# Optimization experiments

Hardware: AMD Instinct MI355X
Metric: run time of the kernel (lower is better)

The kernel has to match this reference:

```python
import jax, jax.numpy as jnp
import numpy as np

EMBED = 512
KDIM = 512
VDIM = 512
HEADS = 8
DHEAD = EMBED // HEADS  # 64
SCALE = 1.0 / np.sqrt(DHEAD).astype(np.float32)


def setup_inputs() -> dict:
    key = jax.random.key(0)
    ks = jax.random.split(key, 11)
    B, Lq, Lk = 4, 2048, 2048
    s_in = 1.0 / np.sqrt(EMBED).astype(np.float32)
    return {
        "query": jax.random.normal(ks[0], (B, Lq, EMBED), jnp.float32),
        "key": jax.random.normal(ks[1], (B, Lk, KDIM), jnp.float32),
        "value": jax.random.normal(ks[2], (B, Lk, VDIM), jnp.float32),
        "wq": jax.random.normal(ks[3], (EMBED, KDIM), jnp.float32) * s_in,
        "bq": jnp.zeros((KDIM,), jnp.float32),
        "wk": jax.random.normal(ks[4], (KDIM, KDIM), jnp.float32) * s_in,
        "bk": jnp.zeros((KDIM,), jnp.float32),
        "wv": jax.random.normal(ks[5], (VDIM, VDIM), jnp.float32) * s_in,
        "bv": jnp.zeros((VDIM,), jnp.float32),
        "wo": jax.random.normal(ks[6], (VDIM, EMBED), jnp.float32) * s_in,
        "bo": jnp.zeros((EMBED,), jnp.float32),
    }


def _split_heads(x):
    b, l, _ = x.shape
    return x.reshape(b, l, HEADS, DHEAD).transpose(0, 2, 1, 3)  # b h l d


def reference(query, key, value, wq, bq, wk, bk, wv, bv, wo, bo):
    # Linear projections (weights stored [in, out])
    q = _split_heads(query @ wq + bq)   # b h Lq d
    k = _split_heads(key @ wk + bk)     # b h Lk d
    v = _split_heads(value @ wv + bv)   # b h Lk d
    scores = jnp.einsum('bhid,bhjd->bhij', q, k) * SCALE  # b h Lq Lk
    attn = jax.nn.softmax(scores, axis=-1)
    # dropout is identity in eval mode
    ctx = jnp.einsum('bhij,bhjd->bhid', attn, v)  # b h Lq d
    b, h, l, d = ctx.shape
    ctx = ctx.transpose(0, 2, 1, 3).reshape(b, l, h * d)  # b Lq vdim
    return ctx @ wo + bo
```

## Files before the change

### kernel.cpp

```cpp
#include <hip/hip_runtime.h>
#include <stdint.h>

typedef unsigned short u16;
typedef unsigned int u32;
typedef __attribute__((ext_vector_type(8))) short short8;
typedef __attribute__((ext_vector_type(4))) float f32x4;
typedef __attribute__((ext_vector_type(16))) float f32x16;

#define DEVI static __device__ __forceinline__

DEVI u16 f2bf(float f) {
  union { float f; u32 u; } v; v.f = f;
  u32 r = v.u + 0x7FFFu + ((v.u >> 16) & 1u);
  return (u16)(r >> 16);
}

DEVI u32 pack2bf(float lo, float hi) {
  return (u32)f2bf(lo) | ((u32)f2bf(hi) << 16);
}

DEVI u32 pack2bf_fast(float lo, float hi) {
  union { float f; u32 u; } a, b;
  a.f = lo; b.f = hi;
  return __builtin_amdgcn_perm(b.u + 0x8000u, a.u + 0x8000u, 0x07060302u);
}

DEVI u32 sum2bf(u32 a, u32 b, float sc) {
  union { u32 u; float f; } alo, ahi, blo, bhi;
  alo.u = a << 16; ahi.u = a & 0xFFFF0000u;
  blo.u = b << 16; bhi.u = b & 0xFFFF0000u;
  return pack2bf_fast((alo.f + blo.f) * sc, (ahi.f + bhi.f) * sc);
}

DEVI void gload_lds16(const u16* g, u16* l) {
  __builtin_amdgcn_global_load_lds((const __attribute__((address_space(1))) void*)g,
                                   (__attribute__((address_space(3))) void*)l, 16, 0, 0);
}

DEVI int sw8(int chunk, int r) { return ((chunk ^ (r & 7) ^ ((r >> 3) & 3)) * 8); }

__global__ __launch_bounds__(256) void tw4(const float* __restrict__ s0, const float* __restrict__ s1,
                                           const float* __restrict__ s2, const float* __restrict__ s3,
                                           u16* __restrict__ d0, u16* __restrict__ d1,
                                           u16* __restrict__ d2, u16* __restrict__ d3) {
  int z = blockIdx.z;
  const float* src = z == 0 ? s0 : z == 1 ? s1 : z == 2 ? s2 : s3;
  u16* dst = z == 0 ? d0 : z == 1 ? d1 : z == 2 ? d2 : d3;
  __shared__ float tile[32][33];
  int tx = threadIdx.x & 31, ty = threadIdx.x >> 5;
  int bx = blockIdx.x * 32, by = blockIdx.y * 32;
#pragma unroll
  for (int i = 0; i < 32; i += 8)
    tile[ty + i][tx] = src[(size_t)(by + ty + i) * 512 + bx + tx];
  __syncthreads();
#pragma unroll
  for (int i = 0; i < 32; i += 8)
    dst[(size_t)(bx + ty + i) * 512 + by + tx] = f2bf(tile[tx][ty + i]);
}

__global__ __launch_bounds__(256) void gemm_qkv(
    const float* __restrict__ A0, const float* __restrict__ A1, const float* __restrict__ A2,
    const u16* __restrict__ W0, const u16* __restrict__ W1, const u16* __restrict__ W2,
    const float* __restrict__ b0, const float* __restrict__ b1, const float* __restrict__ b2,
    u16* __restrict__ oq, u16* __restrict__ ok, u16* __restrict__ vt, float qscale) {
  const int z = blockIdx.z;
  const float* A = z == 0 ? A0 : z == 1 ? A1 : A2;
  const u16* WT = z == 0 ? W0 : z == 1 ? W1 : W2;
  const float* bias = z == 0 ? b0 : z == 1 ? b1 : b2;
  const float sc = z == 0 ? qscale : 1.0f;

  __shared__ __align__(16) u16 smem[128 * 64 * 2];
  u16* As = smem;
  u16* Bs = smem + 128 * 64;
  const int t = threadIdx.x;
  const int w = t >> 6, lane = t & 63, quad = lane >> 4, li = lane & 15;
  const int flat = blockIdx.x + (blockIdx.y << 2);
  const int xcd = flat & 7, idx = flat >> 3;
  const int m0 = (((idx >> 2) << 3) + xcd) * 128;
  const int n0 = (idx & 3) * 128;
  const int wm = (w >> 1) * 64, wn = (w & 1) * 64;

  f32x4 zv = {0.f, 0.f, 0.f, 0.f};
  f32x4 acc[4][4];
#pragma unroll
  for (int mi = 0; mi < 4; mi++)
#pragma unroll
    for (int ni = 0; ni < 4; ni++) acc[mi][ni] = zv;

  const int rA = t >> 3, cA = t & 7;
  for (int it = 0; it < 8; it++) {
    const int k0 = it * 64;
#pragma unroll
    for (int p = 0; p < 4; p++) {
      int r = p * 32 + rA;
      const float* ga = A + (size_t)(m0 + r) * 512 + k0 + cA * 8;
      float4 f0 = *(const float4*)ga;
      float4 f1 = *(const float4*)(ga + 4);
      uint4 pk;
      pk.x = pack2bf_fast(f0.x, f0.y);
      pk.y = pack2bf_fast(f0.z, f0.w);
      pk.z = pack2bf_fast(f1.x, f1.y);
      pk.w = pack2bf_fast(f1.z, f1.w);
      *(uint4*)&As[r * 64 + sw8(cA, r)] = pk;
    }
#pragma unroll
    for (int p = 0; p < 4; p++) {
      int s = p * 256 + t;
      int r = s >> 3, c8 = s & 7;
      gload_lds16(WT + (size_t)(n0 + r) * 512 + k0 + sw8(c8, r), &Bs[(p * 256 + w * 64) * 8]);
    }
    __syncthreads();
#pragma unroll
    for (int ks = 0; ks < 2; ks++) {
      short8 af[4], bf[4];
#pragma unroll
      for (int mi = 0; mi < 4; mi++) {
        int r = wm + mi * 16 + li;
        af[mi] = *(const short8*)&As[r * 64 + sw8(ks * 4 + quad, r)];
      }
#pragma unroll
      for (int ni = 0; ni < 4; ni++) {
        int r = wn + ni * 16 + li;
        bf[ni] = *(const short8*)&Bs[r * 64 + sw8(ks * 4 + quad, r)];
      }
#pragma unroll
      for (int mi = 0; mi < 4; mi++)
#pragma unroll
        for (int ni = 0; ni < 4; ni++)
          acc[mi][ni] = __builtin_amdgcn_mfma_f32_16x16x32_bf16(af[mi], bf[ni], acc[mi][ni], 0, 0, 0);
    }
    __syncthreads();
  }

  float bv[4];
#pragma unroll
  for (int ni = 0; ni < 4; ni++) bv[ni] = bias[n0 + wn + ni * 16 + li];

  if (z < 2) {
    u16* out = z == 0 ? oq : ok;
#pragma unroll
    for (int mi = 0; mi < 4; mi++)
#pragma unroll
      for (int ni = 0; ni < 4; ni++)
#pragma unroll
        for (int r = 0; r < 4; r++) {
          int row = m0 + wm + mi * 16 + quad * 4 + r;
          int col = n0 + wn + ni * 16 + li;
          out[(size_t)row * 512 + col] = f2bf((acc[mi][ni][r] + bv[ni]) * sc);
        }
  } else {
    u16* LT = smem;
#pragma unroll
    for (int mi = 0; mi < 4; mi++)
#pragma unroll
      for (int ni = 0; ni < 4; ni++) {
        int col = wn + ni * 16 + li;
        int row0 = wm + mi * 16 + quad * 4;
        uint2 dw;
        dw.x = pack2bf(acc[mi][ni][0] + bv[ni], acc[mi][ni][1] + bv[ni]);
        dw.y = pack2bf(acc[mi][ni][2] + bv[ni], acc[mi][ni][3] + bv[ni]);
        *(uint2*)&LT[col * 128 + (row0 ^ ((col & 7) << 3))] = dw;
      }
    __syncthreads();
    const int rr = t >> 1, half = t & 1;
    const int colg = n0 + rr;
    const int h = colg >> 6, dd = colg & 63;
    const int bb = m0 >> 11, l0 = m0 & 2047;
    u16* gdst = vt + ((size_t)((bb * 8 + h) * 64 + dd)) * 2048 + l0 + half * 64;
#pragma unroll
    for (int c = 0; c < 8; c++) {
      short8 v = *(const short8*)&LT[rr * 128 + half * 64 + ((c ^ (rr & 7)) << 3)];
      *(short8*)(gdst + c * 8) = v;
    }
  }
}

__global__ __launch_bounds__(256) void gemm_out(const u16* __restrict__ O0,
                                                const u16* __restrict__ O1,
                                                const float* __restrict__ Lb,
                                                const u16* __restrict__ WT,
                                                const float* __restrict__ bias,
                                                float* __restrict__ out) {
  __shared__ __align__(16) u16 As[128 * 64];
  __shared__ __align__(16) u16 Bs[64 * 64];
  __shared__ float Linv[8 * 128];
  const int t = threadIdx.x;
  const int w = t >> 6, lane = t & 63, quad = lane >> 4, li = lane & 15;
  const int flat = blockIdx.x + (blockIdx.y << 3);
  const int xcd = flat & 7, idx = flat >> 3;
  const int m0 = (((idx >> 3) << 3) + xcd) * 128;
  const int n0 = (idx & 7) * 64;
  const int wm = (w >> 1) * 64, wn = (w & 1) * 32;
  const int bb = m0 >> 11, qb = m0 & 2047;

#pragma unroll
  for (int j = 0; j < 4; j++) {
    int f2 = t + j * 256;
    int hh = f2 >> 7, qq = f2 & 127;
    float l0v = Lb[((size_t)((bb * 8 + hh) * 2 + 0)) * 2048 + qb + qq];
    float l1v = Lb[((size_t)((bb * 8 + hh) * 2 + 1)) * 2048 + qb + qq];
    Linv[f2] = 1.0f / (l0v + l1v);
  }
  __syncthreads();

  f32x4 zv = {0.f, 0.f, 0.f, 0.f};
  f32x4 acc[4][2];
#pragma unroll
  for (int mi = 0; mi < 4; mi++)
#pragma unroll
    for (int ni = 0; ni < 2; ni++) acc[mi][ni] = zv;

  const int rA = t >> 3, cA = t & 7;
  for (int it = 0; it < 8; it++) {
    const int k0 = it * 64;
#pragma unroll
    for (int p = 0; p < 4; p++) {
      int r = p * 32 + rA;
      size_t off = (size_t)(m0 + r) * 512 + k0 + cA * 8;
      uint4 a0 = *(const uint4*)&O0[off];
      uint4 a1 = *(const uint4*)&O1[off];
      float scq = Linv[it * 128 + r];
      uint4 pk;
      pk.x = sum2bf(a0.x, a1.x, scq);
      pk.y = sum2bf(a0.y, a1.y, scq);
      pk.z = sum2bf(a0.z, a1.z, scq);
      pk.w = sum2bf(a0.w, a1.w, scq);
      *(uint4*)&As[r * 64 + sw8(cA, r)] = pk;
    }
#pragma unroll
    for (int p = 0; p < 2; p++) {
      int s = p * 256 + t;
      int r = s >> 3, c8 = s & 7;
      gload_lds16(WT + (size_t)(n0 + r) * 512 + k0 + sw8(c8, r), &Bs[(p * 256 + w * 64) * 8]);
    }
    __syncthreads();
#pragma unroll
    for (int ks = 0; ks < 2; ks++) {
      short8 af[4], bf[2];
#pragma unroll
      for (int mi = 0; mi < 4; mi++) {
        int r = wm + mi * 16 + li;
        af[mi] = *(const short8*)&As[r * 64 + sw8(ks * 4 + quad, r)];
      }
#pragma unroll
      for (int ni = 0; ni < 2; ni++) {
        int r = wn + ni * 16 + li;
        bf[ni] = *(const short8*)&Bs[r * 64 + sw8(ks * 4 + quad, r)];
      }
#pragma unroll
      for (int mi = 0; mi < 4; mi++)
#pragma unroll
        for (int ni = 0; ni < 2; ni++)
          acc[mi][ni] = __builtin_amdgcn_mfma_f32_16x16x32_bf16(af[mi], bf[ni], acc[mi][ni], 0, 0, 0);
    }
    __syncthreads();
  }

  float bv[2];
#pragma unroll
  for (int ni = 0; ni < 2; ni++) bv[ni] = bias[n0 + wn + ni * 16 + li];
#pragma unroll
  for (int mi = 0; mi < 4; mi++)
#pragma unroll
    for (int ni = 0; ni < 2; ni++)
#pragma unroll
      for (int r = 0; r < 4; r++) {
        int row = m0 + wm + mi * 16 + quad * 4 + r;
        int col = n0 + wn + ni * 16 + li;
        out[(size_t)row * 512 + col] = acc[mi][ni][r] + bv[ni];
      }
}

__global__ __launch_bounds__(256, 4) void attn(const u16* __restrict__ Qp,
                                               const u16* __restrict__ Kp,
                                               const u16* __restrict__ VT,
                                               u16* __restrict__ Oq0,
                                               u16* __restrict__ Oq1,
                                               float* __restrict__ Lb) {
  __shared__ __align__(16) u16 Ks[64 * 64];
  __shared__ __align__(16) u16 Vs[64 * 64];
  __shared__ __align__(16) u16 Ps[4][32 * 64];
  const int t = threadIdx.x;
  const int w = t >> 6, lane = t & 63, qn = lane & 31, hi = lane >> 5;
  const int flat = blockIdx.x + (blockIdx.y << 4);
  const int xcd = flat & 7, idx = flat >> 3;
  const int g = ((idx >> 4) << 3) + xcd;
  const int h = g >> 1, s = g & 1;
  const int b = blockIdx.z;
  const int q0 = (idx & 15) * 128;
  const int qrow = q0 + w * 32 + qn;

  short8 qf[4];
  {
    const u16* qg = Qp + (size_t)(b * 2048 + qrow) * 512 + h * 64 + hi * 8;
#pragma unroll
    for (int ks = 0; ks < 4; ks++) qf[ks] = *(const short8*)(qg + ks * 16);
  }

  f32x16 o[2];
#pragma unroll
  for (int dt = 0; dt < 2; dt++)
#pragma unroll
    for (int r = 0; r < 16; r++) o[dt][r] = 0.f;
  float lsum = 0.f;

  u16* pw = &Ps[w][0];

  for (int kt = s * 16; kt < s * 16 + 16; kt++) {
    const int k0 = kt * 64;
#pragma unroll
    for (int i = 0; i < 2; i++) {
      int si = i * 256 + t;
      int r = si >> 3, c8 = si & 7;
      gload_lds16(Kp + (size_t)(b * 2048 + k0 + r) * 512 + h * 64 + sw8(c8, r),
                  &Ks[(i * 256 + w * 64) * 8]);
      gload_lds16(VT + ((size_t)((b * 8 + h) * 64 + r)) * 2048 + k0 + sw8(c8, r),
                  &Vs[(i * 256 + w * 64) * 8]);
    }
    __syncthreads();

    f32x16 st[2];
#pragma unroll
    for (int kjt = 0; kjt < 2; kjt++) {
#pragma unroll
      for (int r = 0; r < 16; r++) st[kjt][r] = 0.f;
#pragma unroll
      for (int ks = 0; ks < 4; ks++) {
        int m = kjt * 32 + qn;
        short8 ka = *(const short8*)&Ks[m * 64 + sw8(ks * 2 + hi, m)];
        st[kjt] = __builtin_amdgcn_mfma_f32_32x32x16_bf16(ka, qf[ks], st[kjt], 0, 0, 0);
      }
    }

#pragma unroll
    for (int kjt = 0; kjt < 2; kjt++)
#pragma unroll
      for (int k8 = 0; k8 < 4; k8++) {
        float p0 = __builtin_amdgcn_exp2f(st[kjt][k8 * 4 + 0]);
        float p1 = __builtin_amdgcn_exp2f(st[kjt][k8 * 4 + 1]);
        float p2 = __builtin_amdgcn_exp2f(st[kjt][k8 * 4 + 2]);
        float p3 = __builtin_amdgcn_exp2f(st[kjt][k8 * 4 + 3]);
        lsum += (p0 + p1) + (p2 + p3);
        uint2 dw;
        dw.x = pack2bf_fast(p0, p1);
        dw.y = pack2bf_fast(p2, p3);
        *(uint2*)&pw[qn * 64 + sw8(kjt * 4 + k8, qn) + hi * 4] = dw;
      }

    short8 pb[4];
#pragma unroll
    for (int ks = 0; ks < 4; ks++)
      pb[ks] = *(const short8*)&pw[qn * 64 + sw8(ks * 2 + hi, qn)];
#pragma unroll
    for (int dt = 0; dt < 2; dt++)
#pragma unroll
      for (int ks = 0; ks < 4; ks++) {
        int m = dt * 32 + qn;
        short8 va = *(const short8*)&Vs[m * 64 + sw8(ks * 2 + hi, m)];
        o[dt] = __builtin_amdgcn_mfma_f32_32x32x16_bf16(va, pb[ks], o[dt], 0, 0, 0);
      }
    __syncthreads();
  }

  float l = lsum + __shfl_xor(lsum, 32);
  if (hi == 0) Lb[((size_t)((b * 8 + h) * 2 + s)) * 2048 + qrow] = l;
  u16* Oq = s == 0 ? Oq0 : Oq1;
#pragma unroll
  for (int dt = 0; dt < 2; dt++)
#pragma unroll
    for (int k8 = 0; k8 < 4; k8++) {
      uint2 dw;
      dw.x = pack2bf_fast(o[dt][k8 * 4 + 0], o[dt][k8 * 4 + 1]);
      dw.y = pack2bf_fast(o[dt][k8 * 4 + 2], o[dt][k8 * 4 + 3]);
      *(uint2*)&pw[qn * 64 + sw8(dt * 4 + k8, qn) + hi * 4] = dw;
    }
  __builtin_amdgcn_s_waitcnt(0);
  int q = lane >> 1, half = lane & 1;
  u16* dst = Oq + (size_t)(b * 2048 + q0 + w * 32 + q) * 512 + h * 64 + half * 32;
#pragma unroll
  for (int cc = 0; cc < 4; cc++) {
    int chunk = half * 4 + cc;
    *(short8*)(dst + cc * 8) = *(const short8*)&pw[q * 64 + sw8(chunk, q)];
  }
}

extern "C" void kernel_launch(void* const* d_in, const int* in_sizes, int n_in,
                              void* d_out, int out_size, void* d_ws, size_t ws_size,
                              hipStream_t stream) {
  const float* query = (const float*)d_in[0];
  const float* key_ = (const float*)d_in[1];
  const float* value = (const float*)d_in[2];
  const float* wq = (const float*)d_in[3];
  const float* bq = (const float*)d_in[4];
  const float* wk = (const float*)d_in[5];
  const float* bk = (const float*)d_in[6];
  const float* wv = (const float*)d_in[7];
  const float* bv = (const float*)d_in[8];
  const float* wo = (const float*)d_in[9];
  const float* bo = (const float*)d_in[10];

  char* ws = (char*)d_ws;
  const size_t SZ_W = (size_t)512 * 512 * 2;
  const size_t SZ_X = (size_t)8192 * 512 * 2;
  u16* wqT = (u16*)(ws);
  u16* wkT = (u16*)(ws + SZ_W);
  u16* wvT = (u16*)(ws + 2 * SZ_W);
  u16* woT = (u16*)(ws + 3 * SZ_W);
  u16* Qp = (u16*)(ws + 4 * SZ_W);
  u16* Kp = (u16*)(ws + 4 * SZ_W + SZ_X);
  u16* VTp = (u16*)(ws + 4 * SZ_W + 2 * SZ_X);
  u16* Oq0 = (u16*)(ws + 4 * SZ_W + 3 * SZ_X);
  u16* Oq1 = (u16*)(ws + 4 * SZ_W + 4 * SZ_X);
  float* Lb = (float*)(ws + 4 * SZ_W + 5 * SZ_X);

  const float C1 = 0.125f * 1.44269504088896f;

  tw4<<<dim3(16, 16, 4), 256, 0, stream>>>(wq, wk, wv, wo, wqT, wkT, wvT, woT);
  gemm_qkv<<<dim3(4, 64, 3), 256, 0, stream>>>(query, key_, value, wqT, wkT, wvT,
                                               bq, bk, bv, Qp, Kp, VTp, C1);
  attn<<<dim3(16, 16, 4), 256, 0, stream>>>(Qp, Kp, VTp, Oq0, Oq1, Lb);
  gemm_out<<<dim3(8, 64), 256, 0, stream>>>(Oq0, Oq1, Lb, woT, bo, (float*)d_out);
}
```

Baseline: 199.6 us.

## Double queries per attention wave and split keys four ways

Each attention wave now processes two 32-row query sub-tiles against each loaded K/V tile, so every K/V LDS load feeds twice as many MFMAs. The key range is split into four chunks of 512 instead of two of 1024, which keeps the block count the same. The output GEMM now sums four bf16 partial outputs and four row-sum partials per row. The denominator buffer is moved into the start of the workspace, over weight buffers that are already consumed by then. The costs are more partial-output traffic into the output GEMM and higher register pressure, since the occupancy hint in launch bounds was removed.

Result: slower. 221.6 us (+11.0%).

```diff
diff --git a/kernel.cpp b/kernel.cpp
--- a/kernel.cpp
+++ b/kernel.cpp
@@ -25,11 +25,18 @@
   return __builtin_amdgcn_perm(b.u + 0x8000u, a.u + 0x8000u, 0x07060302u);
 }
 
-DEVI u32 sum2bf(u32 a, u32 b, float sc) {
-  union { u32 u; float f; } alo, ahi, blo, bhi;
-  alo.u = a << 16; ahi.u = a & 0xFFFF0000u;
-  blo.u = b << 16; bhi.u = b & 0xFFFF0000u;
-  return pack2bf_fast((alo.f + blo.f) * sc, (ahi.f + bhi.f) * sc);
+DEVI u32 sum4bf(u32 a, u32 b, u32 c, u32 d, float sc) {
+  union { u32 u; float f; } t;
+  float lo, hi;
+  t.u = a << 16; lo = t.f;
+  t.u = b << 16; lo += t.f;
+  t.u = c << 16; lo += t.f;
+  t.u = d << 16; lo += t.f;
+  t.u = a & 0xFFFF0000u; hi = t.f;
+  t.u = b & 0xFFFF0000u; hi += t.f;
+  t.u = c & 0xFFFF0000u; hi += t.f;
+  t.u = d & 0xFFFF0000u; hi += t.f;
+  return pack2bf_fast(lo * sc, hi * sc);
 }
 
 DEVI void gload_lds16(const u16* g, u16* l) {
@@ -175,12 +182,12 @@
   }
 }
 
-__global__ __launch_bounds__(256) void gemm_out(const u16* __restrict__ O0,
-                                                const u16* __restrict__ O1,
+__global__ __launch_bounds__(256) void gemm_out(const u16* __restrict__ Oqs,
                                                 const float* __restrict__ Lb,
                                                 const u16* __restrict__ WT,
                                                 const float* __restrict__ bias,
                                                 float* __restrict__ out) {
+  const size_t OQS = (size_t)4 * 1024 * 1024;
   __shared__ __align__(16) u16 As[128 * 64];
   __shared__ __align__(16) u16 Bs[64 * 64];
   __shared__ float Linv[8 * 128];
@@ -197,9 +204,11 @@
   for (int j = 0; j < 4; j++) {
     int f2 = t + j * 256;
     int hh = f2 >> 7, qq = f2 & 127;
-    float l0v = Lb[((size_t)((bb * 8 + hh) * 2 + 0)) * 2048 + qb + qq];
-    float l1v = Lb[((size_t)((bb * 8 + hh) * 2 + 1)) * 2048 + qb + qq];
-    Linv[f2] = 1.0f / (l0v + l1v);
+    float lsum = 0.f;
+#pragma unroll
+    for (int s = 0; s < 4; s++)
+      lsum += Lb[((size_t)((bb * 8 + hh) * 4 + s)) * 2048 + qb + qq];
+    Linv[f2] = 1.0f / lsum;
   }
   __syncthreads();
 
@@ -217,14 +226,16 @@
     for (int p = 0; p < 4; p++) {
       int r = p * 32 + rA;
       size_t off = (size_t)(m0 + r) * 512 + k0 + cA * 8;
-      uint4 a0 = *(const uint4*)&O0[off];
-      uint4 a1 = *(const uint4*)&O1[off];
+      uint4 a0 = *(const uint4*)&Oqs[off];
+      uint4 a1 = *(const uint4*)&Oqs[off + OQS];
+      uint4 a2 = *(const uint4*)&Oqs[off + 2 * OQS];
+      uint4 a3 = *(const uint4*)&Oqs[off + 3 * OQS];
       float scq = Linv[it * 128 + r];
       uint4 pk;
-      pk.x = sum2bf(a0.x, a1.x, scq);
-      pk.y = sum2bf(a0.y, a1.y, scq);
-      pk.z = sum2bf(a0.z, a1.z, scq);
-      pk.w = sum2bf(a0.w, a1.w, scq);
+      pk.x = sum4bf(a0.x, a1.x, a2.x, a3.x, scq);
+      pk.y = sum4bf(a0.y, a1.y, a2.y, a3.y, scq);
+      pk.z = sum4bf(a0.z, a1.z, a2.z, a3.z, scq);
+      pk.w = sum4bf(a0.w, a1.w, a2.w, a3.w, scq);
       *(uint4*)&As[r * 64 + sw8(cA, r)] = pk;
     }
 #pragma unroll
@@ -271,42 +282,42 @@
       }
 }
 
-__global__ __launch_bounds__(256, 4) void attn(const u16* __restrict__ Qp,
-                                               const u16* __restrict__ Kp,
-                                               const u16* __restrict__ VT,
-                                               u16* __restrict__ Oq0,
-                                               u16* __restrict__ Oq1,
-                                               float* __restrict__ Lb) {
+__global__ __launch_bounds__(256) void attn(const u16* __restrict__ Qp,
+                                            const u16* __restrict__ Kp,
+                                            const u16* __restrict__ VT,
+                                            u16* __restrict__ Oqs,
+                                            float* __restrict__ Lb) {
+  const size_t OQS = (size_t)4 * 1024 * 1024;
   __shared__ __align__(16) u16 Ks[64 * 64];
   __shared__ __align__(16) u16 Vs[64 * 64];
   __shared__ __align__(16) u16 Ps[4][32 * 64];
   const int t = threadIdx.x;
   const int w = t >> 6, lane = t & 63, qn = lane & 31, hi = lane >> 5;
-  const int flat = blockIdx.x + (blockIdx.y << 4);
-  const int xcd = flat & 7, idx = flat >> 3;
-  const int g = ((idx >> 4) << 3) + xcd;
-  const int h = g >> 1, s = g & 1;
+  const int hs = ((blockIdx.y >> 3) << 3) + (blockIdx.x & 7);
+  const int h = hs >> 2, s = hs & 3;
   const int b = blockIdx.z;
-  const int q0 = (idx & 15) * 128;
-  const int qrow = q0 + w * 32 + qn;
-
-  short8 qf[4];
-  {
-    const u16* qg = Qp + (size_t)(b * 2048 + qrow) * 512 + h * 64 + hi * 8;
-#pragma unroll
-    for (int ks = 0; ks < 4; ks++) qf[ks] = *(const short8*)(qg + ks * 16);
-  }
-
-  f32x16 o[2];
-#pragma unroll
-  for (int dt = 0; dt < 2; dt++)
-#pragma unroll
-    for (int r = 0; r < 16; r++) o[dt][r] = 0.f;
-  float lsum = 0.f;
+  const int q0 = (blockIdx.y & 7) * 256;
+
+  short8 qf[2][4];
+#pragma unroll
+  for (int u = 0; u < 2; u++) {
+    const u16* qg = Qp + (size_t)(b * 2048 + q0 + w * 64 + u * 32 + qn) * 512 + h * 64 + hi * 8;
+#pragma unroll
+    for (int ks = 0; ks < 4; ks++) qf[u][ks] = *(const short8*)(qg + ks * 16);
+  }
+
+  f32x16 o[2][2];
+#pragma unroll
+  for (int u = 0; u < 2; u++)
+#pragma unroll
+    for (int dt = 0; dt < 2; dt++)
+#pragma unroll
+      for (int r = 0; r < 16; r++) o[u][dt][r] = 0.f;
+  float lsum[2] = {0.f, 0.f};
 
   u16* pw = &Ps[w][0];
 
-  for (int kt = s * 16; kt < s * 16 + 16; kt++) {
+  for (int kt = s * 8; kt < s * 8 + 8; kt++) {
     const int k0 = kt * 64;
 #pragma unroll
     for (int i = 0; i < 2; i++) {
@@ -319,68 +330,75 @@
     }
     __syncthreads();
 
-    f32x16 st[2];
-#pragma unroll
-    for (int kjt = 0; kjt < 2; kjt++) {
-#pragma unroll
-      for (int r = 0; r < 16; r++) st[kjt][r] = 0.f;
-#pragma unroll
-      for (int ks = 0; ks < 4; ks++) {
-        int m = kjt * 32 + qn;
-        short8 ka = *(const short8*)&Ks[m * 64 + sw8(ks * 2 + hi, m)];
-        st[kjt] = __builtin_amdgcn_mfma_f32_32x32x16_bf16(ka, qf[ks], st[kjt], 0, 0, 0);
-      }
-    }
-
-#pragma unroll
-    for (int kjt = 0; kjt < 2; kjt++)
+#pragma unroll
+    for (int u = 0; u < 2; u++) {
+      f32x16 st[2];
+#pragma unroll
+      for (int kjt = 0; kjt < 2; kjt++) {
+#pragma unroll
+        for (int r = 0; r < 16; r++) st[kjt][r] = 0.f;
+#pragma unroll
+        for (int ks = 0; ks < 4; ks++) {
+          int m = kjt * 32 + qn;
+          short8 ka = *(const short8*)&Ks[m * 64 + sw8(ks * 2 + hi, m)];
+          st[kjt] = __builtin_amdgcn_mfma_f32_32x32x16_bf16(ka, qf[u][ks], st[kjt], 0, 0, 0);
+        }
+      }
+
+#pragma unroll
+      for (int kjt = 0; kjt < 2; kjt++)
+#pragma unroll
+        for (int k8 = 0; k8 < 4; k8++) {
+          float p0 = __builtin_amdgcn_exp2f(st[kjt][k8 * 4 + 0]);
+          float p1 = __builtin_amdgcn_exp2f(st[kjt][k8 * 4 + 1]);
+          float p2 = __builtin_amdgcn_exp2f(st[kjt][k8 * 4 + 2]);
+          float p3 = __builtin_amdgcn_exp2f(st[kjt][k8 * 4 + 3]);
+          lsum[u] += (p0 + p1) + (p2 + p3);
+          uint2 dw;
+          dw.x = pack2bf_fast(p0, p1);
+          dw.y = pack2bf_fast(p2, p3);
+          *(uint2*)&pw[qn * 64 + sw8(kjt * 4 + k8, qn) + hi * 4] = dw;
+        }
+
+      short8 pb[4];
+#pragma unroll
+      for (int ks = 0; ks < 4; ks++)
+        pb[ks] = *(const short8*)&pw[qn * 64 + sw8(ks * 2 + hi, qn)];
+#pragma unroll
+      for (int dt = 0; dt < 2; dt++)
+#pragma unroll
+        for (int ks = 0; ks < 4; ks++) {
+          int m = dt * 32 + qn;
+          short8 va = *(const short8*)&Vs[m * 64 + sw8(ks * 2 + hi, m)];
+          o[u][dt] = __builtin_amdgcn_mfma_f32_32x32x16_bf16(va, pb[ks], o[u][dt], 0, 0, 0);
+        }
+    }
+    __syncthreads();
+  }
+
+  u16* Oq = Oqs + (size_t)s * OQS;
+#pragma unroll
+  for (int u = 0; u < 2; u++) {
+    float l = lsum[u] + __shfl_xor(lsum[u], 32);
+    int qrow = q0 + w * 64 + u * 32 + qn;
+    if (hi == 0) Lb[((size_t)((b * 8 + h) * 4 + s)) * 2048 + qrow] = l;
+#pragma unroll
+    for (int dt = 0; dt < 2; dt++)
 #pragma unroll
       for (int k8 = 0; k8 < 4; k8++) {
-        float p0 = __builtin_amdgcn_exp2f(st[kjt][k8 * 4 + 0]);
-        float p1 = __builtin_amdgcn_exp2f(st[kjt][k8 * 4 + 1]);
-        float p2 = __builtin_amdgcn_exp2f(st[kjt][k8 * 4 + 2]);
-        float p3 = __builtin_amdgcn_exp2f(st[kjt][k8 * 4 + 3]);
-        lsum += (p0 + p1) + (p2 + p3);
         uint2 dw;
-        dw.x = pack2bf_fast(p0, p1);
-        dw.y = pack2bf_fast(p2, p3);
-        *(uint2*)&pw[qn * 64 + sw8(kjt * 4 + k8, qn) + hi * 4] = dw;
-      }
-
-    short8 pb[4];
-#pragma unroll
-    for (int ks = 0; ks < 4; ks++)
-      pb[ks] = *(const short8*)&pw[qn * 64 + sw8(ks * 2 + hi, qn)];
-#pragma unroll
-    for (int dt = 0; dt < 2; dt++)
-#pragma unroll
-      for (int ks = 0; ks < 4; ks++) {
-        int m = dt * 32 + qn;
-        short8 va = *(const short8*)&Vs[m * 64 + sw8(ks * 2 + hi, m)];
-        o[dt] = __builtin_amdgcn_mfma_f32_32x32x16_bf16(va, pb[ks], o[dt], 0, 0, 0);
-      }
-    __syncthreads();
-  }
-
-  float l = lsum + __shfl_xor(lsum, 32);
-  if (hi == 0) Lb[((size_t)((b * 8 + h) * 2 + s)) * 2048 + qrow] = l;
-  u16* Oq = s == 0 ? Oq0 : Oq1;
-#pragma unroll
-  for (int dt = 0; dt < 2; dt++)
-#pragma unroll
-    for (int k8 = 0; k8 < 4; k8++) {
-      uint2 dw;
-      dw.x = pack2bf_fast(o[dt][k8 * 4 + 0], o[dt][k8 * 4 + 1]);
-      dw.y = pack2bf_fast(o[dt][k8 * 4 + 2], o[dt][k8 * 4 + 3]);
-      *(uint2*)&pw[qn * 64 + sw8(dt * 4 + k8, qn) + hi * 4] = dw;
-    }
-  __builtin_amdgcn_s_waitcnt(0);
-  int q = lane >> 1, half = lane & 1;
-  u16* dst = Oq + (size_t)(b * 2048 + q0 + w * 32 + q) * 512 + h * 64 + half * 32;
-#pragma unroll
-  for (int cc = 0; cc < 4; cc++) {
-    int chunk = half * 4 + cc;
-    *(short8*)(dst + cc * 8) = *(const short8*)&pw[q * 64 + sw8(chunk, q)];
+        dw.x = pack2bf_fast(o[u][dt][k8 * 4 + 0], o[u][dt][k8 * 4 + 1]);
+        dw.y = pack2bf_fast(o[u][dt][k8 * 4 + 2], o[u][dt][k8 * 4 + 3]);
+        *(uint2*)&pw[qn * 64 + sw8(dt * 4 + k8, qn) + hi * 4] = dw;
+      }
+    __builtin_amdgcn_s_waitcnt(0);
+    int q = lane >> 1, half = lane & 1;
+    u16* dst = Oq + (size_t)(b * 2048 + q0 + w * 64 + u * 32 + q) * 512 + h * 64 + half * 32;
+#pragma unroll
+    for (int cc = 0; cc < 4; cc++) {
+      int chunk = half * 4 + cc;
+      *(short8*)(dst + cc * 8) = *(const short8*)&pw[q * 64 + sw8(chunk, q)];
+    }
   }
 }
 
@@ -409,15 +427,14 @@
   u16* Qp = (u16*)(ws + 4 * SZ_W);
   u16* Kp = (u16*)(ws + 4 * SZ_W + SZ_X);
   u16* VTp = (u16*)(ws + 4 * SZ_W + 2 * SZ_X);
-  u16* Oq0 = (u16*)(ws + 4 * SZ_W + 3 * SZ_X);
-  u16* Oq1 = (u16*)(ws + 4 * SZ_W + 4 * SZ_X);
-  float* Lb = (float*)(ws + 4 * SZ_W + 5 * SZ_X);
+  u16* Oqs = (u16*)(ws + 4 * SZ_W + 3 * SZ_X);
+  float* Lb = (float*)(ws);
 
   const float C1 = 0.125f * 1.44269504088896f;
 
   tw4<<<dim3(16, 16, 4), 256, 0, stream>>>(wq, wk, wv, wo, wqT, wkT, wvT, woT);
   gemm_qkv<<<dim3(4, 64, 3), 256, 0, stream>>>(query, key_, value, wqT, wkT, wvT,
                                                bq, bk, bv, Qp, Kp, VTp, C1);
-  attn<<<dim3(16, 16, 4), 256, 0, stream>>>(Qp, Kp, VTp, Oq0, Oq1, Lb);
-  gemm_out<<<dim3(8, 64), 256, 0, stream>>>(Oq0, Oq1, Lb, woT, bo, (float*)d_out);
-}
+  attn<<<dim3(8, 32, 4), 256, 0, stream>>>(Qp, Kp, VTp, Oqs, Lb);
+  gemm_out<<<dim3(8, 64), 256, 0, stream>>>(Oqs, Lb, woT, bo, (float*)d_out);
+}
```

## Replace direct-to-LDS loads with register prefetch double buffering in GEMMs and attention

Applied to the files above, without the earlier changes.

Replaces global_load_lds async copies in the QKV GEMM, output GEMM and attention kernels with register prefetch of the next K-tile. Each tile is written to LDS from registers while the following tile's global loads are in flight. The barriers now wait only on LDS counters, so outstanding global loads can overlap the MFMA work. The weight transpose kernel also moves to 64x64 tiles with vectorized float4 loads and uint2 stores. This costs extra registers and explicit LDS store instructions, which may reduce occupancy.

Measured after the change: 249.0 us. 24.7% more time.

```diff
diff --git a/kernel.cpp b/kernel.cpp
--- a/kernel.cpp
+++ b/kernel.cpp
@@ -32,9 +32,9 @@
   return pack2bf_fast((alo.f + blo.f) * sc, (ahi.f + bhi.f) * sc);
 }
 
-DEVI void gload_lds16(const u16* g, u16* l) {
-  __builtin_amdgcn_global_load_lds((const __attribute__((address_space(1))) void*)g,
-                                   (__attribute__((address_space(3))) void*)l, 16, 0, 0);
+DEVI void barrier_lds() {
+  __builtin_amdgcn_s_waitcnt(0xC07F);
+  __builtin_amdgcn_s_barrier();
 }
 
 DEVI int sw8(int chunk, int r) { return ((chunk ^ (r & 7) ^ ((r >> 3) & 3)) * 8); }
@@ -46,16 +46,28 @@
   int z = blockIdx.z;
   const float* src = z == 0 ? s0 : z == 1 ? s1 : z == 2 ? s2 : s3;
   u16* dst = z == 0 ? d0 : z == 1 ? d1 : z == 2 ? d2 : d3;
-  __shared__ float tile[32][33];
-  int tx = threadIdx.x & 31, ty = threadIdx.x >> 5;
-  int bx = blockIdx.x * 32, by = blockIdx.y * 32;
-#pragma unroll
-  for (int i = 0; i < 32; i += 8)
-    tile[ty + i][tx] = src[(size_t)(by + ty + i) * 512 + bx + tx];
+  __shared__ float tile[64 * 65];
+  const int t = threadIdx.x;
+  const int bx = blockIdx.x * 64, by = blockIdx.y * 64;
+  const int r = t >> 4, c4 = (t & 15) * 4;
+#pragma unroll
+  for (int i = 0; i < 4; i++) {
+    int rr = r + i * 16;
+    float4 v = *(const float4*)&src[(size_t)(by + rr) * 512 + bx + c4];
+    tile[rr * 65 + c4 + 0] = v.x;
+    tile[rr * 65 + c4 + 1] = v.y;
+    tile[rr * 65 + c4 + 2] = v.z;
+    tile[rr * 65 + c4 + 3] = v.w;
+  }
   __syncthreads();
 #pragma unroll
-  for (int i = 0; i < 32; i += 8)
-    dst[(size_t)(bx + ty + i) * 512 + by + tx] = f2bf(tile[tx][ty + i]);
+  for (int i = 0; i < 4; i++) {
+    int rr = r + i * 16;
+    uint2 dw;
+    dw.x = pack2bf(tile[(c4 + 0) * 65 + rr], tile[(c4 + 1) * 65 + rr]);
+    dw.y = pack2bf(tile[(c4 + 2) * 65 + rr], tile[(c4 + 3) * 65 + rr]);
+    *(uint2*)&dst[(size_t)(bx + rr) * 512 + by + c4] = dw;
+  }
 }
 
 __global__ __launch_bounds__(256) void gemm_qkv(
@@ -88,28 +100,46 @@
     for (int ni = 0; ni < 4; ni++) acc[mi][ni] = zv;
 
   const int rA = t >> 3, cA = t & 7;
+  const int sB = t, rB = sB >> 3, c8B = sB & 7;
+
+  float4 apf[4][2];
+  uint4 bpf[4];
+#pragma unroll
+  for (int p = 0; p < 4; p++) {
+    int r = p * 32 + rA;
+    const float* ga = A + (size_t)(m0 + r) * 512 + cA * 8;
+    apf[p][0] = *(const float4*)ga;
+    apf[p][1] = *(const float4*)(ga + 4);
+    int s = p * 256 + t, rb = s >> 3, c8 = s & 7;
+    bpf[p] = *(const uint4*)&WT[(size_t)(n0 + rb) * 512 + sw8(c8, rb)];
+  }
+
   for (int it = 0; it < 8; it++) {
-    const int k0 = it * 64;
 #pragma unroll
     for (int p = 0; p < 4; p++) {
       int r = p * 32 + rA;
-      const float* ga = A + (size_t)(m0 + r) * 512 + k0 + cA * 8;
-      float4 f0 = *(const float4*)ga;
-      float4 f1 = *(const float4*)(ga + 4);
       uint4 pk;
-      pk.x = pack2bf_fast(f0.x, f0.y);
-      pk.y = pack2bf_fast(f0.z, f0.w);
-      pk.z = pack2bf_fast(f1.x, f1.y);
-      pk.w = pack2bf_fast(f1.z, f1.w);
+      pk.x = pack2bf_fast(apf[p][0].x, apf[p][0].y);
+      pk.y = pack2bf_fast(apf[p][0].z, apf[p][0].w);
+      pk.z = pack2bf_fast(apf[p][1].x, apf[p][1].y);
+      pk.w = pack2bf_fast(apf[p][1].z, apf[p][1].w);
       *(uint4*)&As[r * 64 + sw8(cA, r)] = pk;
-    }
-#pragma unroll
-    for (int p = 0; p < 4; p++) {
       int s = p * 256 + t;
-      int r = s >> 3, c8 = s & 7;
-      gload_lds16(WT + (size_t)(n0 + r) * 512 + k0 + sw8(c8, r), &Bs[(p * 256 + w * 64) * 8]);
-    }
-    __syncthreads();
+      *(uint4*)&Bs[s * 8] = bpf[p];
+    }
+    if (it < 7) {
+      const int k0 = (it + 1) * 64;
+#pragma unroll
+      for (int p = 0; p < 4; p++) {
+        int r = p * 32 + rA;
+        const float* ga = A + (size_t)(m0 + r) * 512 + k0 + cA * 8;
+        apf[p][0] = *(const float4*)ga;
+        apf[p][1] = *(const float4*)(ga + 4);
+        int s = p * 256 + t, rb = s >> 3, c8 = s & 7;
+        bpf[p] = *(const uint4*)&WT[(size_t)(n0 + rb) * 512 + k0 + sw8(c8, rb)];
+      }
+    }
+    barrier_lds();
 #pragma unroll
     for (int ks = 0; ks < 2; ks++) {
       short8 af[4], bf[4];
@@ -129,7 +159,7 @@
         for (int ni = 0; ni < 4; ni++)
           acc[mi][ni] = __builtin_amdgcn_mfma_f32_16x16x32_bf16(af[mi], bf[ni], acc[mi][ni], 0, 0, 0);
     }
-    __syncthreads();
+    barrier_lds();
   }
 
   float bv[4];
@@ -211,29 +241,54 @@
     for (int ni = 0; ni < 2; ni++) acc[mi][ni] = zv;
 
   const int rA = t >> 3, cA = t & 7;
+
+  uint4 a0pf[4], a1pf[4], bpf[2];
+#pragma unroll
+  for (int p = 0; p < 4; p++) {
+    int r = p * 32 + rA;
+    size_t off = (size_t)(m0 + r) * 512 + cA * 8;
+    a0pf[p] = *(const uint4*)&O0[off];
+    a1pf[p] = *(const uint4*)&O1[off];
+  }
+#pragma unroll
+  for (int p = 0; p < 2; p++) {
+    int s = p * 256 + t, rb = s >> 3, c8 = s & 7;
+    bpf[p] = *(const uint4*)&WT[(size_t)(n0 + rb) * 512 + sw8(c8, rb)];
+  }
+
   for (int it = 0; it < 8; it++) {
-    const int k0 = it * 64;
 #pragma unroll
     for (int p = 0; p < 4; p++) {
       int r = p * 32 + rA;
-      size_t off = (size_t)(m0 + r) * 512 + k0 + cA * 8;
-      uint4 a0 = *(const uint4*)&O0[off];
-      uint4 a1 = *(const uint4*)&O1[off];
       float scq = Linv[it * 128 + r];
       uint4 pk;
-      pk.x = sum2bf(a0.x, a1.x, scq);
-      pk.y = sum2bf(a0.y, a1.y, scq);
-      pk.z = sum2bf(a0.z, a1.z, scq);
-      pk.w = sum2bf(a0.w, a1.w, scq);
+      pk.x = sum2bf(a0pf[p].x, a1pf[p].x, scq);
+      pk.y = sum2bf(a0pf[p].y, a1pf[p].y, scq);
+      pk.z = sum2bf(a0pf[p].z, a1pf[p].z, scq);
+      pk.w = sum2bf(a0pf[p].w, a1pf[p].w, scq);
       *(uint4*)&As[r * 64 + sw8(cA, r)] = pk;
     }
 #pragma unroll
     for (int p = 0; p < 2; p++) {
       int s = p * 256 + t;
-      int r = s >> 3, c8 = s & 7;
-      gload_lds16(WT + (size_t)(n0 + r) * 512 + k0 + sw8(c8, r), &Bs[(p * 256 + w * 64) * 8]);
-    }
-    __syncthreads();
+      *(uint4*)&Bs[s * 8] = bpf[p];
+    }
+    if (it < 7) {
+      const int k0 = (it + 1) * 64;
+#pragma unroll
+      for (int p = 0; p < 4; p++) {
+        int r = p * 32 + rA;
+        size_t off = (size_t)(m0 + r) * 512 + k0 + cA * 8;
+        a0pf[p] = *(const uint4*)&O0[off];
+        a1pf[p] = *(const uint4*)&O1[off];
+      }
+#pragma unroll
+      for (int p = 0; p < 2; p++) {
+        int s = p * 256 + t, rb = s >> 3, c8 = s & 7;
+        bpf[p] = *(const uint4*)&WT[(size_t)(n0 + rb) * 512 + k0 + sw8(c8, rb)];
+      }
+    }
+    barrier_lds();
 #pragma unroll
     for (int ks = 0; ks < 2; ks++) {
       short8 af[4], bf[2];
@@ -253,7 +308,7 @@
         for (int ni = 0; ni < 2; ni++)
           acc[mi][ni] = __builtin_amdgcn_mfma_f32_16x16x32_bf16(af[mi], bf[ni], acc[mi][ni], 0, 0, 0);
     }
-    __syncthreads();
+    barrier_lds();
   }
 
   float bv[2];
@@ -306,18 +361,31 @@
 
   u16* pw = &Ps[w][0];
 
+  uint4 kpf[2], vpf[2];
+#pragma unroll
+  for (int i = 0; i < 2; i++) {
+    int si = i * 256 + t, r = si >> 3, c8 = si & 7;
+    kpf[i] = *(const uint4*)&Kp[(size_t)(b * 2048 + s * 1024 + r) * 512 + h * 64 + sw8(c8, r)];
+    vpf[i] = *(const uint4*)&VT[((size_t)((b * 8 + h) * 64 + r)) * 2048 + s * 1024 + sw8(c8, r)];
+  }
+
   for (int kt = s * 16; kt < s * 16 + 16; kt++) {
-    const int k0 = kt * 64;
 #pragma unroll
     for (int i = 0; i < 2; i++) {
       int si = i * 256 + t;
-      int r = si >> 3, c8 = si & 7;
-      gload_lds16(Kp + (size_t)(b * 2048 + k0 + r) * 512 + h * 64 + sw8(c8, r),
-                  &Ks[(i * 256 + w * 64) * 8]);
-      gload_lds16(VT + ((size_t)((b * 8 + h) * 64 + r)) * 2048 + k0 + sw8(c8, r),
-                  &Vs[(i * 256 + w * 64) * 8]);
-    }
-    __syncthreads();
+      *(uint4*)&Ks[si * 8] = kpf[i];
+      *(uint4*)&Vs[si * 8] = vpf[i];
+    }
+    if (kt < s * 16 + 15) {
+      const int k0 = (kt + 1) * 64;
+#pragma unroll
+      for (int i = 0; i < 2; i++) {
+        int si = i * 256 + t, r = si >> 3, c8 = si & 7;
+        kpf[i] = *(const uint4*)&Kp[(size_t)(b * 2048 + k0 + r) * 512 + h * 64 + sw8(c8, r)];
+        vpf[i] = *(const uint4*)&VT[((size_t)((b * 8 + h) * 64 + r)) * 2048 + k0 + sw8(c8, r)];
+      }
+    }
+    barrier_lds();
 
     f32x16 st[2];
 #pragma unroll
@@ -359,7 +427,7 @@
         short8 va = *(const short8*)&Vs[m * 64 + sw8(ks * 2 + hi, m)];
         o[dt] = __builtin_amdgcn_mfma_f32_32x32x16_bf16(va, pb[ks], o[dt], 0, 0, 0);
       }
-    __syncthreads();
+    barrier_lds();
   }
 
   float l = lsum + __shfl_xor(lsum, 32);
@@ -415,7 +483,7 @@
 
   const float C1 = 0.125f * 1.44269504088896f;
 
-  tw4<<<dim3(16, 16, 4), 256, 0, stream>>>(wq, wk, wv, wo, wqT, wkT, wvT, woT);
+  tw4<<<dim3(8, 8, 4), 256, 0, stream>>>(wq, wk, wv, wo, wqT, wkT, wvT, woT);
   gemm_qkv<<<dim3(4, 64, 3), 256, 0, stream>>>(query, key_, value, wqT, wkT, wvT,
                                                bq, bk, bv, Qp, Kp, VTp, C1);
   attn<<<dim3(16, 16, 4), 256, 0, stream>>>(Qp, Kp, VTp, Oq0, Oq1, Lb);
```
